# Kernel optimization log

Hardware: AMD Instinct MI355X
Metric: run time of the kernel (lower is better)

## Reference

```python
import jax, jax.numpy as jnp
import numpy as np

MAX_DISP = 20  # matches init_kwargs max_displacement


def setup_inputs() -> dict:
    key = jax.random.key(0)
    k1, k2 = jax.random.split(key)
    feat1 = jax.random.normal(k1, (4, 128, 64, 64), dtype=jnp.float32)
    feat2 = jax.random.normal(k2, (4, 128, 64, 64), dtype=jnp.float32)
    return {"feat1": feat1, "feat2": feat2}


def reference(feat1, feat2):
    pad = MAX_DISP
    D = 2 * pad + 1  # displacement window side (41)
    b, c, h, w = feat1.shape
    feat2_pad = jnp.pad(feat2, ((0, 0), (0, 0), (pad, pad), (pad, pad)))

    def step(carry, ij):
        i = ij // D
        j = ij % D
        sl = jax.lax.dynamic_slice(feat2_pad, (0, 0, i, j), (b, c, h, w))
        # dot over channel dim -> [b, h, w]
        return carry, jnp.sum(feat1 * sl, axis=1)

    # scan over all D*D displacements keeps peak memory at one [b,c,h,w] slice
    _, corr = jax.lax.scan(step, None, jnp.arange(D * D))  # [D*D, b, h, w]
    return jnp.transpose(corr, (1, 0, 2, 3))  # [b, D*D, h, w]
```

## Files before the change

kernel.cpp:

```cpp
#include <hip/hip_runtime.h>
#include <stdint.h>


#define NB 4
#define NC 128
#define NH 64
#define NW 64
#define PAD 20
#define ND 41
#define HW (NH * NW)

typedef __attribute__((ext_vector_type(8))) __bf16 bf16x8;
typedef __attribute__((ext_vector_type(16))) float f32x16;

__device__ __forceinline__ float f4elem(const float4 v, int j) {
  return j == 0 ? v.x : j == 1 ? v.y : j == 2 ? v.z : v.w;
}

__device__ __forceinline__ unsigned int pk2(float a, float b) {
  unsigned short lo = __builtin_bit_cast(unsigned short, (__bf16)a);
  unsigned short hi = __builtin_bit_cast(unsigned short, (__bf16)b);
  return (unsigned int)lo | ((unsigned int)hi << 16);
}

__device__ __forceinline__ void convwrite(const float4 (&v)[8],
                                          uint4* __restrict__ lds, int xq,
                                          int cg) {
#pragma unroll
  for (int j = 0; j < 4; ++j) {
    const int x = xq * 4 + j;
    uint4 u;
    u.x = pk2(f4elem(v[0], j), f4elem(v[1], j));
    u.y = pk2(f4elem(v[2], j), f4elem(v[3], j));
    u.z = pk2(f4elem(v[4], j), f4elem(v[5], j));
    u.w = pk2(f4elem(v[6], j), f4elem(v[7], j));
    lds[x * 16 + (cg ^ (x & 7))] = u;
  }
}

__global__ __launch_bounds__(256, 2) void corr_kernel(
    const float* __restrict__ feat1, const float* __restrict__ feat2,
    float* __restrict__ out) {
  __shared__ uint4 f2s[2][64 * 16];
  __shared__ float cbuf[2][64 * 64];

  const int bid = blockIdx.x;
  const int lid = (bid & 7) * 64 + (bid >> 3);
  const int half = lid & 1;
  const int y = (lid >> 1) & 63;
  const int b = lid >> 7;

  const int t = threadIdx.x;
  const int lane = t & 63;
  const int wv = t >> 6;
  const int I = wv & 1;
  const int J = wv >> 1;

  const int xa = I * 32 + (lane & 31);
  const int xb = J * 32 + (lane & 31);
  const int kh = lane >> 5;
  const int aBase = xa * 16, aSw = xa & 7;
  const int bBase = xb * 16, bSw = xb & 7;
  const int col = (lane & 31) + J * 32;
  const int rbase = kh * 4 + I * 32;

  const int xg = t & 63;
  const int g = t >> 6;

  const int xq = t & 15;
  const int cg = t >> 4;
  const size_t rowoff = (size_t)cg * 8 * HW + xq * 4;
  const float* f1row = feat1 + (size_t)b * NC * HW + (size_t)y * NW + rowoff;
  const float* f2row0 = feat2 + (size_t)b * NC * HW + rowoff;
  const size_t outBase = ((size_t)b * (ND * ND) * NH + y) * NW;

  int dBeg, dEnd;
  if (half == 0) {
    dBeg = (y < PAD) ? (PAD - y) : 0;
    dEnd = PAD + 1;
  } else {
    dBeg = PAD + 1;
    const int e = (NH + PAD) - y;
    dEnd = e < ND ? e : ND;
  }

  const int zBeg = half ? dEnd : 0;
  const int zEnd = half ? ND : dBeg;
  for (int di = zBeg; di < zEnd; ++di) {
    const size_t dB = outBase + (size_t)di * ND * HW;
    for (int k = g; k < ND; k += 4)
      __builtin_nontemporal_store(0.f, &out[dB + (size_t)k * HW + xg]);
  }
  if (dBeg >= dEnd) return;

  float4 v[8];
#pragma unroll
  for (int i = 0; i < 8; ++i) v[i] = *(const float4*)(f1row + (size_t)i * HW);
  uint4* f1tmp = (uint4*)&cbuf[0][0];
  convwrite(v, f1tmp, xq, cg);
  {
    const int yp0 = y + dBeg - PAD;
#pragma unroll
    for (int i = 0; i < 8; ++i)
      v[i] = *(const float4*)(f2row0 + (size_t)yp0 * NW + (size_t)i * HW);
  }
  __syncthreads();
  bf16x8 bfrag[8];
#pragma unroll
  for (int ks = 0; ks < 8; ++ks) {
    const int q = ks * 2 + kh;
    bfrag[ks] = __builtin_bit_cast(bf16x8, f1tmp[bBase + (q ^ bSw)]);
  }
  __syncthreads();

  const int nIter = dEnd - dBeg;
  int p = 0;
#pragma unroll 1
  for (int j = 0; j < nIter; ++j) {
    convwrite(v, f2s[p], xq, cg);
    {
      const int nj = (j + 1 < nIter) ? j + 1 : j;
      const int ypn = y + dBeg + nj - PAD;
#pragma unroll
      for (int i = 0; i < 8; ++i)
        v[i] = *(const float4*)(f2row0 + (size_t)ypn * NW + (size_t)i * HW);
    }
    __syncthreads();

    f32x16 acc;
#pragma unroll
    for (int r = 0; r < 16; ++r) acc[r] = 0.f;
#pragma unroll
    for (int ks = 0; ks < 8; ++ks) {
      const int q = ks * 2 + kh;
      bf16x8 a = __builtin_bit_cast(bf16x8, f2s[p][aBase + (q ^ aSw)]);
      acc = __builtin_amdgcn_mfma_f32_32x32x16_bf16(a, bfrag[ks], acc, 0, 0, 0);
    }
#pragma unroll
    for (int r = 0; r < 16; ++r) {
      const int row = rbase + (r & 3) + 8 * (r >> 2);
      cbuf[p][row * 64 + col] = acc[r];
    }

    if (j > 0) {
      const size_t dBase = outBase + (size_t)(dBeg + j - 1) * ND * HW;
      const float* cb = cbuf[p ^ 1];
      for (int k = g; k < ND; k += 4) {
        const int xs = xg + k - PAD;
        const float vv = (xs >= 0 && xs < NW) ? cb[xs * 64 + xg] : 0.f;
        __builtin_nontemporal_store(vv, &out[dBase + (size_t)k * HW + xg]);
      }
    }
    p ^= 1;
  }

  __syncthreads();
  {
    const size_t dBase = outBase + (size_t)(dEnd - 1) * ND * HW;
    const float* cb = cbuf[p ^ 1];
    for (int k = g; k < ND; k += 4) {
      const int xs = xg + k - PAD;
      const float vv = (xs >= 0 && xs < NW) ? cb[xs * 64 + xg] : 0.f;
      __builtin_nontemporal_store(vv, &out[dBase + (size_t)k * HW + xg]);
    }
  }
}

extern "C" void kernel_launch(void* const* d_in, const int* in_sizes, int n_in,
                              void* d_out, int out_size, void* d_ws,
                              size_t ws_size, hipStream_t stream) {
  (void)in_sizes; (void)n_in; (void)out_size; (void)d_ws; (void)ws_size;
  const float* f1 = (const float*)d_in[0];
  const float* f2 = (const float*)d_in[1];
  float* out = (float*)d_out;
  corr_kernel<<<dim3(NB * NH * 2), dim3(256), 0, stream>>>(f1, f2, out);
}
```

Baseline: 42.25 us.

## Pre-convert features to bf16 MFMA layout in workspace, split displacements four ways

A separate kernel now converts feat1 and feat2 to bf16 once, writing them into a workspace in an MFMA-fragment-friendly layout. The main kernel then loads its A/B fragments straight from global memory, with no per-block fp32 conversion and no staging of feat2 through LDS. The displacement rows are split across four blocks per output row instead of two, with a smaller LDS footprint and higher occupancy. The cost is a second launch and a round trip through the workspace, and the original kernel is kept as a fallback when the workspace is too small.

```diff
diff --git a/kernel.cpp b/kernel.cpp
--- a/kernel.cpp
+++ b/kernel.cpp
@@ -9,18 +9,150 @@
 #define PAD 20
 #define ND 41
 #define HW (NH * NW)
+#define ROW_U4 1024
 
 typedef __attribute__((ext_vector_type(8))) __bf16 bf16x8;
 typedef __attribute__((ext_vector_type(16))) float f32x16;
-
-__device__ __forceinline__ float f4elem(const float4 v, int j) {
-  return j == 0 ? v.x : j == 1 ? v.y : j == 2 ? v.z : v.w;
-}
 
 __device__ __forceinline__ unsigned int pk2(float a, float b) {
   unsigned short lo = __builtin_bit_cast(unsigned short, (__bf16)a);
   unsigned short hi = __builtin_bit_cast(unsigned short, (__bf16)b);
   return (unsigned int)lo | ((unsigned int)hi << 16);
+}
+
+__global__ __launch_bounds__(256) void conv_kernel(
+    const float* __restrict__ f1, const float* __restrict__ f2,
+    uint4* __restrict__ ws) {
+  const int blk = blockIdx.x;
+  const int isF2 = blk >> 8;
+  const int by = blk & 255;
+  const int b = by >> 6, y = by & 63;
+  const float* src = (isF2 ? f2 : f1) + (size_t)b * NC * HW + (size_t)y * NW;
+  uint4* dst = ws + (size_t)isF2 * (NB * NH * ROW_U4) + (size_t)by * ROW_U4;
+  const int x = threadIdx.x & 63;
+  const int cq = threadIdx.x >> 6;
+#pragma unroll
+  for (int it = 0; it < 4; ++it) {
+    const int cg = it * 4 + cq;
+    float v[8];
+#pragma unroll
+    for (int i = 0; i < 8; ++i) v[i] = src[(size_t)(cg * 8 + i) * HW + x];
+    uint4 u;
+    u.x = pk2(v[0], v[1]);
+    u.y = pk2(v[2], v[3]);
+    u.z = pk2(v[4], v[5]);
+    u.w = pk2(v[6], v[7]);
+    dst[cg * 64 + x] = u;
+  }
+}
+
+__global__ __launch_bounds__(256, 4) void corr_main(
+    const uint4* __restrict__ ws, float* __restrict__ out) {
+  __shared__ float cbuf[2][64 * 64];
+
+  const int bid = blockIdx.x;
+  const int lid = (bid & 7) * 128 + (bid >> 3);
+  const int dq = lid & 3;
+  const int y = (lid >> 2) & 63;
+  const int b = lid >> 8;
+
+  const int t = threadIdx.x;
+  const int lane = t & 63;
+  const int wv = t >> 6;
+  const int I = wv & 1;
+  const int J = wv >> 1;
+  const int kh = lane >> 5;
+
+  const int xa = I * 32 + (lane & 31);
+  const int xb = J * 32 + (lane & 31);
+  const int col = (lane & 31) + 32 * J;
+  const int rbase = kh * 4 + I * 32;
+  const int xg = t & 63;
+  const int g = t >> 6;
+
+  const uint4* f1t = ws;
+  const uint4* f2t = ws + NB * NH * ROW_U4;
+
+  const int dBeg = (ND * dq) / 4;
+  const int dEnd = (ND * (dq + 1)) / 4;
+  int a0 = 20 - y;
+  if (a0 < dBeg) a0 = dBeg;
+  if (a0 > dEnd) a0 = dEnd;
+  int a1 = 84 - y;
+  if (a1 < a0) a1 = a0;
+  if (a1 > dEnd) a1 = dEnd;
+
+  const size_t outBase = (size_t)b * (ND * ND) * HW + (size_t)y * NW;
+
+  for (int di = dBeg; di < a0; ++di) {
+    const size_t dB = outBase + (size_t)di * ND * HW;
+    for (int k = g; k < ND; k += 4)
+      __builtin_nontemporal_store(0.f, &out[dB + (size_t)k * HW + xg]);
+  }
+  for (int di = a1; di < dEnd; ++di) {
+    const size_t dB = outBase + (size_t)di * ND * HW;
+    for (int k = g; k < ND; k += 4)
+      __builtin_nontemporal_store(0.f, &out[dB + (size_t)k * HW + xg]);
+  }
+  const int n = a1 - a0;
+  if (n <= 0) return;
+
+  const uint4* f1row = f1t + (size_t)(b * 64 + y) * ROW_U4 + kh * 64 + xb;
+  bf16x8 bfrag[8];
+#pragma unroll
+  for (int ks = 0; ks < 8; ++ks)
+    bfrag[ks] = __builtin_bit_cast(bf16x8, f1row[ks * 128]);
+
+  const uint4* f2row = f2t + (size_t)(b * 64) * ROW_U4 + kh * 64 + xa;
+
+  int p = 0;
+#pragma unroll 1
+  for (int j = 0; j < n; ++j) {
+    const int yp = y + (a0 + j) - PAD;
+    const uint4* ap = f2row + (size_t)yp * ROW_U4;
+    uint4 a[8];
+#pragma unroll
+    for (int ks = 0; ks < 8; ++ks) a[ks] = ap[ks * 128];
+
+    if (j > 0) {
+      const size_t dB = outBase + (size_t)(a0 + j - 1) * ND * HW;
+      const float* cb = cbuf[p ^ 1];
+      for (int k = g; k < ND; k += 4) {
+        const int xs = xg + k - PAD;
+        const float vv = (xs >= 0 && xs < NW) ? cb[xs * 64 + xg] : 0.f;
+        __builtin_nontemporal_store(vv, &out[dB + (size_t)k * HW + xg]);
+      }
+    }
+
+    f32x16 acc;
+#pragma unroll
+    for (int r = 0; r < 16; ++r) acc[r] = 0.f;
+#pragma unroll
+    for (int ks = 0; ks < 8; ++ks)
+      acc = __builtin_amdgcn_mfma_f32_32x32x16_bf16(
+          __builtin_bit_cast(bf16x8, a[ks]), bfrag[ks], acc, 0, 0, 0);
+#pragma unroll
+    for (int r = 0; r < 16; ++r) {
+      const int row = rbase + (r & 3) + 8 * (r >> 2);
+      cbuf[p][row * 64 + col] = acc[r];
+    }
+    __syncthreads();
+    p ^= 1;
+  }
+
+  {
+    const size_t dB = outBase + (size_t)(a0 + n - 1) * ND * HW;
+    const float* cb = cbuf[p ^ 1];
+    for (int k = g; k < ND; k += 4) {
+      const int xs = xg + k - PAD;
+      const float vv = (xs >= 0 && xs < NW) ? cb[xs * 64 + xg] : 0.f;
+      __builtin_nontemporal_store(vv, &out[dB + (size_t)k * HW + xg]);
+    }
+  }
+}
+
+__device__ __forceinline__ float f4elem(const float4 v, int j) {
+  return j == 0 ? v.x : j == 1 ? v.y : j == 2 ? v.z : v.w;
 }
 
 __device__ __forceinline__ void convwrite(const float4 (&v)[8],
@@ -38,7 +170,7 @@
   }
 }
 
-__global__ __launch_bounds__(256, 2) void corr_kernel(
+__global__ __launch_bounds__(256, 2) void corr_fallback(
     const float* __restrict__ feat1, const float* __restrict__ feat2,
     float* __restrict__ out) {
   __shared__ uint4 f2s[2][64 * 16];
@@ -55,7 +187,6 @@
   const int wv = t >> 6;
   const int I = wv & 1;
   const int J = wv >> 1;
-
   const int xa = I * 32 + (lane & 31);
   const int xb = J * 32 + (lane & 31);
   const int kh = lane >> 5;
@@ -63,10 +194,8 @@
   const int bBase = xb * 16, bSw = xb & 7;
   const int col = (lane & 31) + J * 32;
   const int rbase = kh * 4 + I * 32;
-
   const int xg = t & 63;
   const int g = t >> 6;
-
   const int xq = t & 15;
   const int cg = t >> 4;
   const size_t rowoff = (size_t)cg * 8 * HW + xq * 4;
@@ -83,7 +212,6 @@
     const int e = (NH + PAD) - y;
     dEnd = e < ND ? e : ND;
   }
-
   const int zBeg = half ? dEnd : 0;
   const int zEnd = half ? ND : dBeg;
   for (int di = zBeg; di < zEnd; ++di) {
@@ -133,15 +261,14 @@
 #pragma unroll
     for (int ks = 0; ks < 8; ++ks) {
       const int q = ks * 2 + kh;
-      bf16x8 a = __builtin_bit_cast(bf16x8, f2s[p][aBase + (q ^ aSw)]);
-      acc = __builtin_amdgcn_mfma_f32_32x32x16_bf16(a, bfrag[ks], acc, 0, 0, 0);
+      bf16x8 aa = __builtin_bit_cast(bf16x8, f2s[p][aBase + (q ^ aSw)]);
+      acc = __builtin_amdgcn_mfma_f32_32x32x16_bf16(aa, bfrag[ks], acc, 0, 0, 0);
     }
 #pragma unroll
     for (int r = 0; r < 16; ++r) {
       const int row = rbase + (r & 3) + 8 * (r >> 2);
       cbuf[p][row * 64 + col] = acc[r];
     }
-
     if (j > 0) {
       const size_t dBase = outBase + (size_t)(dBeg + j - 1) * ND * HW;
       const float* cb = cbuf[p ^ 1];
@@ -153,7 +280,6 @@
     }
     p ^= 1;
   }
-
   __syncthreads();
   {
     const size_t dBase = outBase + (size_t)(dEnd - 1) * ND * HW;
@@ -169,9 +295,16 @@
 extern "C" void kernel_launch(void* const* d_in, const int* in_sizes, int n_in,
                               void* d_out, int out_size, void* d_ws,
                               size_t ws_size, hipStream_t stream) {
-  (void)in_sizes; (void)n_in; (void)out_size; (void)d_ws; (void)ws_size;
+  (void)in_sizes; (void)n_in; (void)out_size;
   const float* f1 = (const float*)d_in[0];
   const float* f2 = (const float*)d_in[1];
   float* out = (float*)d_out;
-  corr_kernel<<<dim3(NB * NH * 2), dim3(256), 0, stream>>>(f1, f2, out);
-}
+  const size_t need = (size_t)2 * NB * NH * ROW_U4 * sizeof(uint4);
+  if (ws_size >= need && d_ws != nullptr) {
+    uint4* ws = (uint4*)d_ws;
+    conv_kernel<<<dim3(512), dim3(256), 0, stream>>>(f1, f2, ws);
+    corr_main<<<dim3(NB * NH * 4), dim3(256), 0, stream>>>(ws, out);
+  } else {
+    corr_fallback<<<dim3(NB * NH * 2), dim3(256), 0, stream>>>(f1, f2, out);
+  }
+}
```

Measured after the change: 38.13 us. -9.8%, faster.
